# Performance work log

Measured on AMD Instinct MI355X. Metric: run time of the kernel, lower is better.

The kernel has to match this reference:

```python
import jax, jax.numpy as jnp
import numpy as np

C = 256      # n_embd
H = 16       # n_head
HS = C // H  # head_size = 16
B = 64
T = 256      # <= block_size
LN_EPS = 1e-5


def _layer_norm(x, g, b):
    mu = jnp.mean(x, axis=-1, keepdims=True)
    var = jnp.mean((x - mu) ** 2, axis=-1, keepdims=True)
    return (x - mu) * jax.lax.rsqrt(var + LN_EPS) * g + b


def setup_inputs() -> dict:
    key = jax.random.key(0)
    ks = jax.random.split(key, 10)
    s_in = 1.0 / np.sqrt(C)
    s_ff = 1.0 / np.sqrt(4 * C)
    return {
        "x": jax.random.normal(ks[0], (B, T, C), dtype=jnp.float32),
        # per-head Q/K/V weights, stacked: [H, C, HS] (no bias, as in Head)
        "Wq": jax.random.normal(ks[1], (H, C, HS), dtype=jnp.float32) * s_in,
        "Wk": jax.random.normal(ks[2], (H, C, HS), dtype=jnp.float32) * s_in,
        "Wv": jax.random.normal(ks[3], (H, C, HS), dtype=jnp.float32) * s_in,
        "Wp": jax.random.normal(ks[4], (C, C), dtype=jnp.float32) * s_in,
        "bp": jnp.zeros((C,), dtype=jnp.float32),
        "W1": jax.random.normal(ks[5], (C, 4 * C), dtype=jnp.float32) * s_in,
        "b1": jnp.zeros((4 * C,), dtype=jnp.float32),
        "W2": jax.random.normal(ks[6], (4 * C, C), dtype=jnp.float32) * s_ff,
        "b2": jnp.zeros((C,), dtype=jnp.float32),
        "g1": jnp.ones((C,), dtype=jnp.float32),
        "be1": jnp.zeros((C,), dtype=jnp.float32),
        "g2": jnp.ones((C,), dtype=jnp.float32),
        "be2": jnp.zeros((C,), dtype=jnp.float32),
    }


def reference(x, Wq, Wk, Wv, Wp, bp, W1, b1, W2, b2, g1, be1, g2, be2):
    Bx, Tx, Cx = x.shape
    h = _layer_norm(x, g1, be1)
    # per-head projections: [B, H, T, HS]
    q = jnp.einsum('btc,hcd->bhtd', h, Wq)
    k = jnp.einsum('btc,hcd->bhtd', h, Wk)
    v = jnp.einsum('btc,hcd->bhtd', h, Wv)
    # NOTE: original scales by C**-0.5 with C = n_embd, NOT head_size
    scale = 1.0 / np.sqrt(Cx)
    scores = jnp.einsum('bhtd,bhsd->bhts', q, k) * scale
    causal = jnp.tril(jnp.ones((Tx, Tx), dtype=bool))
    scores = jnp.where(causal, scores, -jnp.inf)
    wei = jax.nn.softmax(scores, axis=-1)  # dropout = identity (eval)
    attn = jnp.einsum('bhts,bhsd->bhtd', wei, v)
    # concat heads in order -> [B, T, C]
    attn = attn.transpose(0, 2, 1, 3).reshape(Bx, Tx, Cx)
    attn = attn @ Wp + bp
    x = x + attn
    h2 = _layer_norm(x, g2, be2)
    ffn = jax.nn.gelu(h2 @ W1 + b1, approximate=False) @ W2 + b2
    return x + ffn


if __name__ == "__main__":
    out = reference(**setup_inputs())
    print(out.shape, out.dtype)
```

## Files before the change

kernel.cpp:

```cpp
#include <hip/hip_runtime.h>
#include <hip/hip_bf16.h>

typedef __attribute__((ext_vector_type(8))) short short8;
typedef __attribute__((ext_vector_type(4))) float f32x4;
typedef __attribute__((ext_vector_type(16))) float f32x16;

__device__ __forceinline__ unsigned short f2bf(float f) {
    unsigned u = __float_as_uint(f);
    unsigned r = (u + 0x7fffu + ((u >> 16) & 1u)) >> 16;
    return (unsigned short)r;
}
__device__ __forceinline__ float bf2f(unsigned short h) {
    return __uint_as_float(((unsigned)h) << 16);
}

__device__ __forceinline__ float fast_gelu(float v) {
    float y  = 0.7978845608f * v * (1.0f + 0.044715f * v * v);
    float ay = fabsf(y);
    float e  = __expf(2.0f * ay);
    float th = 1.0f - 2.0f / (e + 1.0f);
    th = __builtin_copysignf(th, y);
    return 0.5f * v * (1.0f + th);
}

__device__ __forceinline__ void gload16(const unsigned short* g, unsigned short* l) {
    __builtin_amdgcn_global_load_lds(
        (const __attribute__((address_space(1))) unsigned int*)g,
        (__attribute__((address_space(3))) unsigned int*)l,
        16, 0, 0);
}

template<int N> __device__ __forceinline__ void vmwait() {
    asm volatile("s_waitcnt vmcnt(%0)" :: "n"(N) : "memory");
}
__device__ __forceinline__ void pipe_barrier() {
    asm volatile("s_waitcnt lgkmcnt(0)" ::: "memory");
    __builtin_amdgcn_s_barrier();
    asm volatile("" ::: "memory");
}

__global__ __launch_bounds__(256) void prep_ln1(
    const float* __restrict__ Wq, const float* __restrict__ Wk,
    const float* __restrict__ Wv, const float* __restrict__ Wp,
    const float* __restrict__ W1, const float* __restrict__ W2,
    unsigned short* __restrict__ WqkvT, unsigned short* __restrict__ WpT,
    unsigned short* __restrict__ W1T, unsigned short* __restrict__ W2T,
    const float* __restrict__ xin, const float* __restrict__ gw,
    const float* __restrict__ bw, unsigned short* __restrict__ h1)
{
    __shared__ float smem[4096];
    const int bid = blockIdx.x, t = threadIdx.x;
    if (bid >= 624) {
        int row  = (bid - 624) * 4 + (t >> 6);
        int lane = t & 63;
        const float4 v = *reinterpret_cast<const float4*>(xin + (size_t)row * 256 + lane * 4);
        float s  = v.x + v.y + v.z + v.w;
        float sq = v.x*v.x + v.y*v.y + v.z*v.z + v.w*v.w;
#pragma unroll
        for (int m = 1; m < 64; m <<= 1) { s += __shfl_xor(s, m); sq += __shfl_xor(sq, m); }
        float mean = s * (1.0f/256.0f);
        float var  = sq * (1.0f/256.0f) - mean*mean;
        float rstd = rsqrtf(var + 1e-5f);
        const float4 g4 = *reinterpret_cast<const float4*>(gw + lane*4);
        const float4 b4 = *reinterpret_cast<const float4*>(bw + lane*4);
        ushort4 o;
        o.x = f2bf((v.x-mean)*rstd*g4.x + b4.x);
        o.y = f2bf((v.y-mean)*rstd*g4.y + b4.y);
        o.z = f2bf((v.z-mean)*rstd*g4.z + b4.z);
        o.w = f2bf((v.w-mean)*rstd*g4.w + b4.w);
        *reinterpret_cast<ushort4*>(h1 + (size_t)row*256 + lane*4) = o;
        return;
    }
    if (bid < 576) {
        const float* W; unsigned short* WT; int N, K, tile0;
        if (bid < 64)       { W = Wp; WT = WpT; N = 256;  K = 256;  tile0 = bid; }
        else if (bid < 320) { W = W1; WT = W1T; N = 1024; K = 256;  tile0 = bid - 64; }
        else                { W = W2; WT = W2T; N = 256;  K = 1024; tile0 = bid - 320; }
        int ntx = N >> 5;
        int bx = tile0 % ntx, by = tile0 / ntx;
        int c0 = bx*32, r0 = by*32;
        int tx = t & 31, ty = t >> 5;
#pragma unroll
        for (int i = 0; i < 4; ++i)
            smem[(ty + i*8)*33 + tx] = W[(size_t)(r0 + ty + i*8)*N + c0 + tx];
        __syncthreads();
#pragma unroll
        for (int i = 0; i < 4; ++i)
            WT[(size_t)(c0 + ty + i*8)*K + r0 + tx] = f2bf(smem[tx*33 + ty + i*8]);
    } else {
        int pb = bid - 576;
        int proj = pb >> 4, hh = pb & 15;
        const float* W = (proj == 0) ? Wq : ((proj == 1) ? Wk : Wv);
        float scale = (proj == 0) ? 0.0625f : 1.0f;
        const float4* src = reinterpret_cast<const float4*>(W + hh*4096);
#pragma unroll
        for (int i = 0; i < 4; ++i) {
            float4 v4 = src[t + i*256];
            *reinterpret_cast<float4*>(&smem[(t + i*256)*4]) = v4;
        }
        __syncthreads();
        int d = t >> 4, cp = (t & 15) * 16;
        unsigned short obuf[16];
#pragma unroll
        for (int i = 0; i < 16; ++i)
            obuf[i] = f2bf(smem[(cp + i)*16 + d] * scale);
        unsigned short* dst = WqkvT + (size_t)(proj*256 + hh*16 + d)*256 + cp;
        *reinterpret_cast<ushort4*>(dst)      = *reinterpret_cast<ushort4*>(&obuf[0]);
        *reinterpret_cast<ushort4*>(dst + 4)  = *reinterpret_cast<ushort4*>(&obuf[4]);
        *reinterpret_cast<ushort4*>(dst + 8)  = *reinterpret_cast<ushort4*>(&obuf[8]);
        *reinterpret_cast<ushort4*>(dst + 12) = *reinterpret_cast<ushort4*>(&obuf[12]);
    }
}

template<int NBX>
__device__ __forceinline__ void swz_bid(int& bx, int& by) {
    int nwg = gridDim.x;
    int bid = blockIdx.x;
    int vid = (bid & 7) * (nwg >> 3) + (bid >> 3);
    bx = vid % NBX;
    by = vid / NBX;
}

template<int BM, int BN, int K>
__device__ __forceinline__ void gemm_core(
    const unsigned short* __restrict__ A, const unsigned short* __restrict__ BT,
    int bx, int by, f32x4 (&acc)[BM/32][BN/32])
{
    constexpr int FM = BM/32, FN = BN/32, NT = K/32;
    constexpr int LA = BM/64, LB = BN/64, L = LA + LB;
    __shared__ unsigned short As[3][BM*32];
    __shared__ unsigned short Bs[3][BN*32];
    const int tid = threadIdx.x, lane = tid & 63, wid = tid >> 6;
    const int wr = (wid >> 1) * (BM/2), wc = (wid & 1) * (BN/2);
    const int c16 = lane & 15, g16 = lane >> 4;
    const int lr = lane >> 2, lq = lane & 3;

#pragma unroll
    for (int m = 0; m < FM; ++m)
#pragma unroll
        for (int n = 0; n < FN; ++n) acc[m][n] = f32x4{0.f, 0.f, 0.f, 0.f};

    const unsigned short* a0 = A  + (size_t)(by*BM + lr)*K + lq*8;
    const unsigned short* b0 = BT + (size_t)(bx*BN + lr)*K + lq*8;

    auto stage = [&](int buf, int t) {
        int k0 = t * 32;
#pragma unroll
        for (int i = 0; i < LA; ++i) {
            int ch = wid*LA + i;
            gload16(a0 + (size_t)ch*16*K + k0, &As[buf][ch*512]);
        }
#pragma unroll
        for (int i = 0; i < LB; ++i) {
            int ch = wid*LB + i;
            gload16(b0 + (size_t)ch*16*K + k0, &Bs[buf][ch*512]);
        }
    };

    auto compute = [&](int buf) {
        short8 af[FM], bf[FN];
#pragma unroll
        for (int m = 0; m < FM; ++m)
            af[m] = *reinterpret_cast<const short8*>(&As[buf][(wr + m*16 + c16)*32 + g16*8]);
#pragma unroll
        for (int n = 0; n < FN; ++n)
            bf[n] = *reinterpret_cast<const short8*>(&Bs[buf][(wc + n*16 + c16)*32 + g16*8]);
#pragma unroll
        for (int m = 0; m < FM; ++m)
#pragma unroll
            for (int n = 0; n < FN; ++n)
                acc[m][n] = __builtin_amdgcn_mfma_f32_16x16x32_bf16(af[m], bf[n], acc[m][n], 0, 0, 0);
    };

    stage(0, 0);
    stage(1, 1);
    int cur = 0;
    for (int t = 0; t < NT - 1; ++t) {
        vmwait<L>();
        pipe_barrier();
        if (t + 2 < NT) {
            int nb = cur + 2; if (nb >= 3) nb -= 3;
            stage(nb, t + 2);
        }
        compute(cur);
        ++cur; if (cur == 3) cur = 0;
    }
    vmwait<0>();
    pipe_barrier();
    compute(cur);
}

template<int BM, int BN, int K>
__device__ __forceinline__ void gemm_core8(
    const unsigned short* __restrict__ A, const unsigned short* __restrict__ BT,
    int bx, int by, f32x4 (&acc)[BM/32][BN/64])
{
    constexpr int FM = BM/32, FN = BN/64, NT = K/32;
    constexpr int NCHA = BM/16, NCH = BM/16 + BN/16;
    constexpr int NR = (NCH + 7) / 8;
    constexpr int NFULL = NCH / 8, NREM = NCH % 8;
    __shared__ unsigned short As[3][BM*32];
    __shared__ unsigned short Bs[3][BN*32];
    const int tid = threadIdx.x, lane = tid & 63, wid = tid >> 6;
    const int wm = wid >> 2, wn = wid & 3;
    const int c16 = lane & 15, g16 = lane >> 4;
    const int lr = lane >> 2, lq = lane & 3;

#pragma unroll
    for (int m = 0; m < FM; ++m)
#pragma unroll
        for (int n = 0; n < FN; ++n) acc[m][n] = f32x4{0.f, 0.f, 0.f, 0.f};

    const unsigned short* a0 = A  + (size_t)(by*BM + lr)*K + lq*8;
    const unsigned short* b0 = BT + (size_t)(bx*BN + lr)*K + lq*8;

    auto stage = [&](int buf, int t) {
        int k0 = t * 32;
#pragma unroll
        for (int i = 0; i < NR; ++i) {
            int ch = i*8 + wid;
            if (ch < NCHA)
                gload16(a0 + (size_t)ch*16*K + k0, &As[buf][ch*512]);
            else if (ch < NCH)
                gload16(b0 + (size_t)(ch-NCHA)*16*K + k0, &Bs[buf][(ch-NCHA)*512]);
        }
    };

    auto compute = [&](int buf) {
        short8 af[FM], bf[FN];
#pragma unroll
        for (int m = 0; m < FM; ++m)
            af[m] = *reinterpret_cast<const short8*>(&As[buf][(wm*(BM/2) + m*16 + c16)*32 + g16*8]);
#pragma unroll
        for (int n = 0; n < FN; ++n)
            bf[n] = *reinterpret_cast<const short8*>(&Bs[buf][(wn*(BN/4) + n*16 + c16)*32 + g16*8]);
#pragma unroll
        for (int m = 0; m < FM; ++m)
#pragma unroll
            for (int n = 0; n < FN; ++n)
                acc[m][n] = __builtin_amdgcn_mfma_f32_16x16x32_bf16(af[m], bf[n], acc[m][n], 0, 0, 0);
    };

    stage(0, 0);
    stage(1, 1);
    int cur = 0;
    for (int t = 0; t < NT - 1; ++t) {
        if constexpr (NREM == 0) {
            vmwait<NFULL>();
        } else {
            if (wid < NREM) vmwait<NFULL + 1>();
            else            vmwait<NFULL>();
        }
        pipe_barrier();
        if (t + 2 < NT) {
            int nb = cur + 2; if (nb >= 3) nb -= 3;
            stage(nb, t + 2);
        }
        compute(cur);
        ++cur; if (cur == 3) cur = 0;
    }
    vmwait<0>();
    pipe_barrier();
    compute(cur);
}

__global__ __launch_bounds__(256) void gemm_qkv(
    const unsigned short* __restrict__ A, const unsigned short* __restrict__ BT,
    unsigned short* __restrict__ qb, unsigned short* __restrict__ kb,
    unsigned short* __restrict__ vtb)
{
    int bx, by; swz_bid<6>(bx, by);
    f32x4 acc[4][4];
    gemm_core<128, 128, 256>(A, BT, bx, by, acc);
    const int lane = threadIdx.x & 63, wid = threadIdx.x >> 6;
    const int c16 = lane & 15, g16 = lane >> 4;
    const int wr = (wid >> 1) * 64, wc = (wid & 1) * 64;
#pragma unroll
    for (int m = 0; m < 4; ++m)
#pragma unroll
    for (int n = 0; n < 4; ++n)
#pragma unroll
    for (int j = 0; j < 4; ++j) {
        int row = by*128 + wr + m*16 + g16*4 + j;
        int col = bx*128 + wc + n*16 + c16;
        int proj = col >> 8, hh = (col >> 4) & 15, dd = col & 15;
        int b = row >> 8, t = row & 255;
        unsigned short val = f2bf(acc[m][n][j]);
        size_t bh = (size_t)(b*16 + hh);
        if (proj == 0)      qb[(bh*256 + t)*16 + dd] = val;
        else if (proj == 1) kb[(bh*256 + t)*16 + dd] = val;
        else                vtb[(bh*16 + dd)*256 + t] = val;
    }
}

__global__ __launch_bounds__(512) void gemm_wp_ln(
    const unsigned short* __restrict__ A, const unsigned short* __restrict__ BT,
    const float* __restrict__ bp, const float* __restrict__ x,
    const float* __restrict__ g2, const float* __restrict__ be2,
    unsigned short* __restrict__ x2b, unsigned short* __restrict__ h2)
{
    int bx, by; swz_bid<1>(bx, by);
    f32x4 acc[2][4];
    gemm_core8<64, 256, 256>(A, BT, 0, by, acc);

    __shared__ float rs[64][4];
    __shared__ float rq[64][4];
    const int tid = threadIdx.x, lane = tid & 63, wid = tid >> 6;
    const int c16 = lane & 15, g16 = lane >> 4;
    const int wm = wid >> 2, wn = wid & 3;

    float vv[2][4][4];
#pragma unroll
    for (int m = 0; m < 2; ++m)
#pragma unroll
    for (int n = 0; n < 4; ++n)
#pragma unroll
    for (int j = 0; j < 4; ++j) {
        int row = by*64 + wm*32 + m*16 + g16*4 + j;
        int col = wn*64 + n*16 + c16;
        size_t idx = (size_t)row*256 + col;
        float v = acc[m][n][j] + bp[col] + x[idx];
        vv[m][n][j] = v;
        x2b[idx] = f2bf(v);
    }
#pragma unroll
    for (int m = 0; m < 2; ++m)
#pragma unroll
    for (int j = 0; j < 4; ++j) {
        float ps = vv[m][0][j] + vv[m][1][j] + vv[m][2][j] + vv[m][3][j];
        float pq = vv[m][0][j]*vv[m][0][j] + vv[m][1][j]*vv[m][1][j]
                 + vv[m][2][j]*vv[m][2][j] + vv[m][3][j]*vv[m][3][j];
#pragma unroll
        for (int mask = 1; mask < 16; mask <<= 1) {
            ps += __shfl_xor(ps, mask);
            pq += __shfl_xor(pq, mask);
        }
        if (c16 == 0) {
            int r = wm*32 + m*16 + g16*4 + j;
            rs[r][wn] = ps;
            rq[r][wn] = pq;
        }
    }
    __syncthreads();
#pragma unroll
    for (int m = 0; m < 2; ++m)
#pragma unroll
    for (int j = 0; j < 4; ++j) {
        int r = wm*32 + m*16 + g16*4 + j;
        float s = rs[r][0] + rs[r][1] + rs[r][2] + rs[r][3];
        float q = rq[r][0] + rq[r][1] + rq[r][2] + rq[r][3];
        float mean = s * (1.0f/256.0f);
        float var  = q * (1.0f/256.0f) - mean*mean;
        float rstd = rsqrtf(var + 1e-5f);
        int row = by*64 + r;
#pragma unroll
        for (int n = 0; n < 4; ++n) {
            int col = wn*64 + n*16 + c16;
            h2[(size_t)row*256 + col] = f2bf((vv[m][n][j]-mean)*rstd*g2[col] + be2[col]);
        }
    }
}

__global__ __launch_bounds__(512) void gemm_ffn1(
    const unsigned short* __restrict__ A, const unsigned short* __restrict__ BT,
    const float* __restrict__ b1, unsigned short* __restrict__ ffh)
{
    int bx, by; swz_bid<4>(bx, by);
    f32x4 acc[4][4];
    gemm_core8<128, 256, 256>(A, BT, bx, by, acc);
    const int lane = threadIdx.x & 63, wid = threadIdx.x >> 6;
    const int c16 = lane & 15, g16 = lane >> 4;
    const int wm = wid >> 2, wn = wid & 3;
#pragma unroll
    for (int m = 0; m < 4; ++m)
#pragma unroll
    for (int n = 0; n < 4; ++n)
#pragma unroll
    for (int j = 0; j < 4; ++j) {
        int row = by*128 + wm*64 + m*16 + g16*4 + j;
        int col = bx*256 + wn*64 + n*16 + c16;
        float v = acc[m][n][j] + b1[col];
        ffh[(size_t)row*1024 + col] = f2bf(fast_gelu(v));
    }
}

__global__ __launch_bounds__(512) void gemm_ffn2(
    const unsigned short* __restrict__ A, const unsigned short* __restrict__ BT,
    const float* __restrict__ b2, const unsigned short* __restrict__ x2b,
    float* __restrict__ out)
{
    int bx, by; swz_bid<1>(bx, by);
    f32x4 acc[1][4];
    gemm_core8<32, 256, 1024>(A, BT, 0, by, acc);
    const int lane = threadIdx.x & 63, wid = threadIdx.x >> 6;
    const int c16 = lane & 15, g16 = lane >> 4;
    const int wm = wid >> 2, wn = wid & 3;
#pragma unroll
    for (int n = 0; n < 4; ++n)
#pragma unroll
    for (int j = 0; j < 4; ++j) {
        int row = by*32 + wm*16 + g16*4 + j;
        int col = wn*64 + n*16 + c16;
        size_t idx = (size_t)row*256 + col;
        out[idx] = acc[0][n][j] + b2[col] + bf2f(x2b[idx]);
    }
}

__global__ __launch_bounds__(256) void attn_kernel(
    const unsigned short* __restrict__ qb, const unsigned short* __restrict__ kb,
    const unsigned short* __restrict__ vtb, unsigned short* __restrict__ ao)
{
    const int bid  = blockIdx.x;
    const int half = bid & 1, h = (bid >> 1) & 15, b = bid >> 5;
    const int tid  = threadIdx.x;
    const int w    = tid >> 6, lane = tid & 63;
    const int l31  = lane & 31, hi = lane >> 5;
    const int chunk = half*4 + w;
    const int t0    = chunk * 32;
    const unsigned short* qh = qb  + (size_t)(b*16 + h) * 4096;
    const unsigned short* kh = kb  + (size_t)(b*16 + h) * 4096;
    const unsigned short* vh = vtb + (size_t)(b*16 + h) * 4096;

    short8 qf = *reinterpret_cast<const short8*>(qh + (size_t)(t0 + l31)*16 + hi*8);

    f32x16 zf, pv;
#pragma unroll
    for (int i = 0; i < 16; ++i) { zf[i] = 0.f; pv[i] = 0.f; }
    float sum = 0.f;
    const int dref = l31 & 15;

    for (int tt = 0; tt <= chunk; ++tt) {
        short8 kf = *reinterpret_cast<const short8*>(kh + (size_t)(tt*32 + l31)*16 + hi*8);
        f32x16 S = __builtin_amdgcn_mfma_f32_32x32x16_bf16(kf, qf, zf, 0, 0, 0);

        float p[16];
#pragma unroll
        for (int r = 0; r < 16; ++r) {
            float pe = __expf(S[r]);
            if (tt == chunk) {
                int s_local = (r & 3) + 8*(r >> 2) + 4*hi;
                pe = (s_local <= l31) ? pe : 0.f;
            }
            p[r] = pe;
            sum += pe;
        }

        unsigned qd[8], xd[8];
#pragma unroll
        for (int i = 0; i < 8; ++i) {
            unsigned rr;
            asm("v_cvt_pk_bf16_f32 %0, %1, %2" : "=v"(rr) : "v"(p[2*i]), "v"(p[2*i+1]));
            qd[i] = rr;
        }
#pragma unroll
        for (int i = 0; i < 8; ++i) xd[i] = (unsigned)__shfl_xor((int)qd[i], 32);

        int4 flo, fhi;
        flo.x = hi ? (int)xd[2] : (int)qd[0];
        flo.y = hi ? (int)xd[3] : (int)qd[1];
        flo.z = hi ? (int)qd[2] : (int)xd[0];
        flo.w = hi ? (int)qd[3] : (int)xd[1];
        fhi.x = hi ? (int)xd[6] : (int)qd[4];
        fhi.y = hi ? (int)xd[7] : (int)qd[5];
        fhi.z = hi ? (int)qd[6] : (int)xd[4];
        fhi.w = hi ? (int)qd[7] : (int)xd[5];
        short8 plo = __builtin_bit_cast(short8, flo);
        short8 phi = __builtin_bit_cast(short8, fhi);

        short8 vf0 = *reinterpret_cast<const short8*>(vh + (size_t)dref*256 + tt*32 + hi*8);
        short8 vf1 = *reinterpret_cast<const short8*>(vh + (size_t)dref*256 + tt*32 + 16 + hi*8);
        pv = __builtin_amdgcn_mfma_f32_32x32x16_bf16(vf0, plo, pv, 0, 0, 0);
        pv = __builtin_amdgcn_mfma_f32_32x32x16_bf16(vf1, phi, pv, 0, 0, 0);
    }

    sum += __shfl_xor(sum, 32);
    float rinv = 1.0f / sum;

    unsigned o0, o1, o2, o3;
    {
        float a0 = pv[0]*rinv, a1 = pv[1]*rinv, a2 = pv[2]*rinv, a3 = pv[3]*rinv;
        float a4 = pv[4]*rinv, a5 = pv[5]*rinv, a6 = pv[6]*rinv, a7 = pv[7]*rinv;
        asm("v_cvt_pk_bf16_f32 %0, %1, %2" : "=v"(o0) : "v"(a0), "v"(a1));
        asm("v_cvt_pk_bf16_f32 %0, %1, %2" : "=v"(o1) : "v"(a2), "v"(a3));
        asm("v_cvt_pk_bf16_f32 %0, %1, %2" : "=v"(o2) : "v"(a4), "v"(a5));
        asm("v_cvt_pk_bf16_f32 %0, %1, %2" : "=v"(o3) : "v"(a6), "v"(a7));
    }
    unsigned short* orow = ao + (size_t)(b*256 + t0 + l31)*256 + h*16;
    uint2 s01 = {o0, o1}, s23 = {o2, o3};
    *reinterpret_cast<uint2*>(orow + hi*4)     = s01;
    *reinterpret_cast<uint2*>(orow + 8 + hi*4) = s23;
}

extern "C" void kernel_launch(void* const* d_in, const int* in_sizes, int n_in,
                              void* d_out, int out_size, void* d_ws, size_t ws_size,
                              hipStream_t stream)
{
    const float* x   = (const float*)d_in[0];
    const float* Wq  = (const float*)d_in[1];
    const float* Wk  = (const float*)d_in[2];
    const float* Wv  = (const float*)d_in[3];
    const float* Wp  = (const float*)d_in[4];
    const float* bp  = (const float*)d_in[5];
    const float* W1  = (const float*)d_in[6];
    const float* b1  = (const float*)d_in[7];
    const float* W2  = (const float*)d_in[8];
    const float* b2  = (const float*)d_in[9];
    const float* g1  = (const float*)d_in[10];
    const float* be1 = (const float*)d_in[11];
    const float* g2  = (const float*)d_in[12];
    const float* be2 = (const float*)d_in[13];
    float* out = (float*)d_out;

    char* ws = (char*)d_ws;
    unsigned short* h1    = (unsigned short*)(ws);
    unsigned short* WqkvT = (unsigned short*)(ws +  8388608);
    unsigned short* WpT   = (unsigned short*)(ws +  8781824);
    unsigned short* W1T   = (unsigned short*)(ws +  8912896);
    unsigned short* W2T   = (unsigned short*)(ws +  9437184);
    unsigned short* qb    = (unsigned short*)(ws +  9961472);
    unsigned short* kb    = (unsigned short*)(ws + 18350080);
    unsigned short* vtb   = (unsigned short*)(ws + 26738688);
    unsigned short* ao    = (unsigned short*)(ws + 35127296);
    unsigned short* ffh   = qb;
    unsigned short* x2b   = (unsigned short*)(ws + 43515904);
    unsigned short* h2    = (unsigned short*)(ws + 60293120);

    prep_ln1<<<4720, 256, 0, stream>>>(Wq, Wk, Wv, Wp, W1, W2,
                                       WqkvT, WpT, W1T, W2T, x, g1, be1, h1);
    gemm_qkv<<<768, 256, 0, stream>>>(h1, WqkvT, qb, kb, vtb);
    attn_kernel<<<2048, 256, 0, stream>>>(qb, kb, vtb, ao);
    gemm_wp_ln<<<256, 512, 0, stream>>>(ao, WpT, bp, x, g2, be2, x2b, h2);
    gemm_ffn1<<<512, 512, 0, stream>>>(h2, W1T, b1, ffh);
    gemm_ffn2<<<512, 512, 0, stream>>>(ffh, W2T, b2, x2b, out);
}
```

Before: 113.4 us.

## Fuse FFN up and down GEMMs into one register-resident kernel

```diff
diff --git a/kernel.cpp b/kernel.cpp
--- a/kernel.cpp
+++ b/kernel.cpp
@@ -361,48 +361,103 @@
     }
 }
 
-__global__ __launch_bounds__(512) void gemm_ffn1(
-    const unsigned short* __restrict__ A, const unsigned short* __restrict__ BT,
-    const float* __restrict__ b1, unsigned short* __restrict__ ffh)
-{
-    int bx, by; swz_bid<4>(bx, by);
-    f32x4 acc[4][4];
-    gemm_core8<128, 256, 256>(A, BT, bx, by, acc);
-    const int lane = threadIdx.x & 63, wid = threadIdx.x >> 6;
-    const int c16 = lane & 15, g16 = lane >> 4;
-    const int wm = wid >> 2, wn = wid & 3;
-#pragma unroll
-    for (int m = 0; m < 4; ++m)
-#pragma unroll
-    for (int n = 0; n < 4; ++n)
-#pragma unroll
-    for (int j = 0; j < 4; ++j) {
-        int row = by*128 + wm*64 + m*16 + g16*4 + j;
-        int col = bx*256 + wn*64 + n*16 + c16;
-        float v = acc[m][n][j] + b1[col];
-        ffh[(size_t)row*1024 + col] = f2bf(fast_gelu(v));
-    }
-}
-
-__global__ __launch_bounds__(512) void gemm_ffn2(
-    const unsigned short* __restrict__ A, const unsigned short* __restrict__ BT,
+__global__ __launch_bounds__(256) void ffn_reg(
+    const unsigned short* __restrict__ h2, const unsigned short* __restrict__ W1T,
+    const unsigned short* __restrict__ W2T, const float* __restrict__ b1,
     const float* __restrict__ b2, const unsigned short* __restrict__ x2b,
     float* __restrict__ out)
 {
-    int bx, by; swz_bid<1>(bx, by);
-    f32x4 acc[1][4];
-    gemm_core8<32, 256, 1024>(A, BT, 0, by, acc);
-    const int lane = threadIdx.x & 63, wid = threadIdx.x >> 6;
-    const int c16 = lane & 15, g16 = lane >> 4;
-    const int wm = wid >> 2, wn = wid & 3;
-#pragma unroll
-    for (int n = 0; n < 4; ++n)
-#pragma unroll
-    for (int j = 0; j < 4; ++j) {
-        int row = by*32 + wm*16 + g16*4 + j;
-        int col = wn*64 + n*16 + c16;
-        size_t idx = (size_t)row*256 + col;
-        out[idx] = acc[0][n][j] + b2[col] + bf2f(x2b[idx]);
+    __shared__ float red[32][257];
+    const int tid = threadIdx.x, w = tid >> 6, lane = tid & 63;
+    const int l31 = lane & 31, hi = lane >> 5;
+    const int row0 = blockIdx.x * 32;
+    const int r = row0 + l31;
+
+    short8 hf[16];
+#pragma unroll
+    for (int kc = 0; kc < 16; ++kc)
+        hf[kc] = *reinterpret_cast<const short8*>(h2 + (size_t)r*256 + kc*16 + hi*8);
+
+    f32x16 zf;
+#pragma unroll
+    for (int i = 0; i < 16; ++i) zf[i] = 0.f;
+    f32x16 acc[8];
+#pragma unroll
+    for (int ct = 0; ct < 8; ++ct) acc[ct] = zf;
+
+    for (int hc = w*8; hc < w*8 + 8; ++hc) {
+        f32x16 S = zf;
+#pragma unroll
+        for (int kc = 0; kc < 16; ++kc) {
+            short8 w1f = *reinterpret_cast<const short8*>(
+                W1T + (size_t)(hc*32 + l31)*256 + kc*16 + hi*8);
+            S = __builtin_amdgcn_mfma_f32_32x32x16_bf16(w1f, hf[kc], S, 0, 0, 0);
+        }
+        float bv = b1[hc*32 + l31];
+        float p[16];
+#pragma unroll
+        for (int r_ = 0; r_ < 16; ++r_) {
+            int pat = (r_ & 3) + 8*(r_ >> 2) + 4*hi;
+            float v = S[r_] + __shfl(bv, pat);
+            p[r_] = fast_gelu(v);
+        }
+        unsigned qd[8], xd[8];
+#pragma unroll
+        for (int i = 0; i < 8; ++i) {
+            unsigned rr;
+            asm("v_cvt_pk_bf16_f32 %0, %1, %2" : "=v"(rr) : "v"(p[2*i]), "v"(p[2*i+1]));
+            qd[i] = rr;
+        }
+#pragma unroll
+        for (int i = 0; i < 8; ++i) xd[i] = (unsigned)__shfl_xor((int)qd[i], 32);
+
+        int4 flo, fhi;
+        flo.x = hi ? (int)xd[2] : (int)qd[0];
+        flo.y = hi ? (int)xd[3] : (int)qd[1];
+        flo.z = hi ? (int)qd[2] : (int)xd[0];
+        flo.w = hi ? (int)qd[3] : (int)xd[1];
+        fhi.x = hi ? (int)xd[6] : (int)qd[4];
+        fhi.y = hi ? (int)xd[7] : (int)qd[5];
+        fhi.z = hi ? (int)qd[6] : (int)xd[4];
+        fhi.w = hi ? (int)qd[7] : (int)xd[5];
+        short8 plo = __builtin_bit_cast(short8, flo);
+        short8 phi = __builtin_bit_cast(short8, fhi);
+
+#pragma unroll
+        for (int ct = 0; ct < 8; ++ct) {
+            const unsigned short* w2p = W2T + (size_t)(ct*32 + l31)*1024 + hc*32;
+            short8 w2f0 = *reinterpret_cast<const short8*>(w2p + hi*8);
+            short8 w2f1 = *reinterpret_cast<const short8*>(w2p + 16 + hi*8);
+            acc[ct] = __builtin_amdgcn_mfma_f32_32x32x16_bf16(w2f0, plo, acc[ct], 0, 0, 0);
+            acc[ct] = __builtin_amdgcn_mfma_f32_32x32x16_bf16(w2f1, phi, acc[ct], 0, 0, 0);
+        }
+    }
+
+    for (int ww = 0; ww < 4; ++ww) {
+        if (w == ww) {
+#pragma unroll
+            for (int ct = 0; ct < 8; ++ct)
+#pragma unroll
+            for (int r_ = 0; r_ < 16; ++r_) {
+                int col = ct*32 + (r_ & 3) + 8*(r_ >> 2) + 4*hi;
+                if (ww == 0) red[l31][col] = acc[ct][r_];
+                else         red[l31][col] += acc[ct][r_];
+            }
+        }
+        __syncthreads();
+    }
+
+    const int er = tid >> 3, ec0 = (tid & 7) * 32;
+#pragma unroll
+    for (int i = 0; i < 8; ++i) {
+        int c = ec0 + i*4;
+        size_t idx = (size_t)(row0 + er)*256 + c;
+        float4 o;
+        o.x = red[er][c+0] + b2[c+0] + bf2f(x2b[idx+0]);
+        o.y = red[er][c+1] + b2[c+1] + bf2f(x2b[idx+1]);
+        o.z = red[er][c+2] + b2[c+2] + bf2f(x2b[idx+2]);
+        o.w = red[er][c+3] + b2[c+3] + bf2f(x2b[idx+3]);
+        *reinterpret_cast<float4*>(out + idx) = o;
     }
 }
 
@@ -521,7 +576,6 @@
     unsigned short* kb    = (unsigned short*)(ws + 18350080);
     unsigned short* vtb   = (unsigned short*)(ws + 26738688);
     unsigned short* ao    = (unsigned short*)(ws + 35127296);
-    unsigned short* ffh   = qb;
     unsigned short* x2b   = (unsigned short*)(ws + 43515904);
     unsigned short* h2    = (unsigned short*)(ws + 60293120);
 
@@ -530,6 +584,5 @@
     gemm_qkv<<<768, 256, 0, stream>>>(h1, WqkvT, qb, kb, vtb);
     attn_kernel<<<2048, 256, 0, stream>>>(qb, kb, vtb, ao);
     gemm_wp_ln<<<256, 512, 0, stream>>>(ao, WpT, bp, x, g2, be2, x2b, h2);
-    gemm_ffn1<<<512, 512, 0, stream>>>(h2, W1T, b1, ffh);
-    gemm_ffn2<<<512, 512, 0, stream>>>(ffh, W2T, b2, x2b, out);
-}
+    ffn_reg<<<512, 256, 0, stream>>>(h2, W1T, W2T, b1, b2, x2b, out);
+}
```

New measurement: 176.7 us. +55.7%, slower.
